# Kernel optimization log

Measured on AMD Instinct MI355X. Metric: run time of the kernel, lower is better.

The kernel has to match this reference:

```python
import jax, jax.numpy as jnp
import numpy as np

N = 40000   # nodes
E = 600000  # edges
G = 64      # graphs
DIN = 128   # input feature dim
H = 128     # hidden_channels
L = 3       # num_layers


def setup_inputs() -> dict:
    key = jax.random.key(0)
    ks = jax.random.split(key, 16)
    s = 0.05
    inp = {}
    inp["x"] = jax.random.normal(ks[0], (N, DIN), jnp.float32)
    inp["edge_attr"] = jax.random.normal(ks[1], (E,), jnp.float32)
    inp["node_w"] = jax.random.normal(ks[2], (DIN, H), jnp.float32) * s
    inp["node_b"] = jnp.zeros((H,), jnp.float32)
    inp["edge_w"] = jax.random.normal(ks[3], (1, H), jnp.float32) * s
    inp["edge_b"] = jnp.zeros((H,), jnp.float32)
    inp["t"] = jnp.ones((L,), jnp.float32)  # learn_t init 1.0
    inp["lin1_w"] = jax.random.normal(ks[4], (L, H, 2 * H), jnp.float32) * s
    inp["lin1_b"] = jnp.zeros((L, 2 * H), jnp.float32)
    inp["ln1_g"] = jnp.ones((L, 2 * H), jnp.float32)
    inp["ln1_bt"] = jnp.zeros((L, 2 * H), jnp.float32)
    inp["lin2_w"] = jax.random.normal(ks[5], (L, 2 * H, H), jnp.float32) * s
    inp["lin2_b"] = jnp.zeros((L, H), jnp.float32)
    inp["blk_g"] = jnp.ones((L, H), jnp.float32)
    inp["blk_b"] = jnp.zeros((L, H), jnp.float32)
    inp["hw1"] = jax.random.normal(ks[6], (H, H // 2), jnp.float32) * s
    inp["hb1"] = jnp.zeros((H // 2,), jnp.float32)
    inp["hw2"] = jax.random.normal(ks[7], (H // 2, H // 4), jnp.float32) * s
    inp["hb2"] = jnp.zeros((H // 4,), jnp.float32)
    inp["hw3"] = jax.random.normal(ks[8], (H // 4, 1), jnp.float32) * s
    inp["hb3"] = jnp.zeros((1,), jnp.float32)
    inp["edge_index"] = jax.random.randint(ks[9], (2, E), 0, N, jnp.int32)
    inp["batch"] = jnp.sort(jax.random.randint(ks[10], (N,), 0, G, jnp.int32))
    return inp


def _layer_norm(v, g, b):
    mu = jnp.mean(v, axis=-1, keepdims=True)
    var = jnp.var(v, axis=-1, keepdims=True)
    return (v - mu) * jax.lax.rsqrt(var + 1e-5) * g + b


def reference(x, edge_attr, node_w, node_b, edge_w, edge_b, t,
              lin1_w, lin1_b, ln1_g, ln1_bt, lin2_w, lin2_b,
              blk_g, blk_b, hw1, hb1, hw2, hb2, hw3, hb3,
              edge_index, batch):
    src, dst = edge_index[0], edge_index[1]
    h = x @ node_w + node_b                       # [N, H]
    ea = edge_attr[:, None] @ edge_w + edge_b     # [E, H]

    def genconv(xn, i):
        # message: relu(x_j + e) + eps
        msg = jax.nn.relu(xn[src] + ea) + 1e-7    # [E, H]
        # scatter-softmax over dst with learnable temperature t
        logit = msg * t[i]
        m = jax.ops.segment_max(logit, dst, num_segments=N)
        m = jnp.where(jnp.isfinite(m), m, 0.0)    # isolated nodes
        ex = jnp.exp(logit - m[dst])
        den = jax.ops.segment_sum(ex, dst, num_segments=N)
        agg = jax.ops.segment_sum(ex * msg, dst, num_segments=N) / jnp.maximum(den, 1e-16)
        o = agg + xn                              # add root
        # GENConv MLP: Linear(H,2H) -> LayerNorm -> ReLU -> Linear(2H,H)
        o = jax.nn.relu(_layer_norm(o @ lin1_w[i] + lin1_b[i], ln1_g[i], ln1_bt[i]))
        return o @ lin2_w[i] + lin2_b[i]

    # layer 0: bare conv (as in the torch forward)
    h = genconv(h, 0)
    # layers 1..L-1: DeepGCNLayer res+ (norm -> act -> [dropout=id in eval] -> conv -> residual)
    for i in range(1, L):
        r = jax.nn.relu(_layer_norm(h, blk_g[i], blk_b[i]))
        h = h + genconv(r, i)
    # final norm+act uses layer 0's norm/act
    h = jax.nn.relu(_layer_norm(h, blk_g[0], blk_b[0]))
    # global mean pool over graphs
    cnt = jax.ops.segment_sum(jnp.ones((N,), h.dtype), batch, num_segments=G)
    pooled = jax.ops.segment_sum(h, batch, num_segments=G) / jnp.maximum(cnt, 1.0)[:, None]
    # MLP head (dropout = identity in eval)
    o = jax.nn.relu(pooled @ hw1 + hb1)
    o = jax.nn.relu(o @ hw2 + hb2)
    return o @ hw3 + hb3                          # [G, 1]
```

## Files before the change

kernel.cpp:

```cpp
#include <hip/hip_runtime.h>
#include <math.h>

#define NN 40000
#define NE 600000
#define NG 64
#define DIM_IN 128
#define HH 128
#define HH2 256

using half8 = __attribute__((ext_vector_type(8))) _Float16;
using half4 = __attribute__((ext_vector_type(4))) _Float16;
using h2    = __attribute__((ext_vector_type(2))) _Float16;
using f4    = __attribute__((ext_vector_type(4))) float;

__device__ __forceinline__ int lower_bound_dev(const int* a, int n, int key) {
    int lo = 0, hi = n;
    while (lo < hi) { int mid = (lo + hi) >> 1; if (a[mid] < key) lo = mid + 1; else hi = mid; }
    return lo;
}

#define NX (NN*DIM_IN)
#define NX4 (NX/4)
__global__ void convert_kernel(const float* __restrict__ x, const float* __restrict__ node_w,
                               const float* __restrict__ lin1_w, const float* __restrict__ lin2_w,
                               _Float16* __restrict__ xh, _Float16* __restrict__ nwt,
                               _Float16* __restrict__ w1t, _Float16* __restrict__ w2t)
{
    int id = blockIdx.x * blockDim.x + threadIdx.x;
    if (id < NX4) {
        float4 v = *(const float4*)(x + (size_t)id * 4);
        half4 o; o.x = (_Float16)v.x; o.y = (_Float16)v.y; o.z = (_Float16)v.z; o.w = (_Float16)v.w;
        *(half4*)(xh + (size_t)id * 4) = o;
        return;
    }
    id -= NX4;
    if (id < 16384) { int n = id >> 7, k = id & 127; nwt[id] = (_Float16)node_w[k*128 + n]; return; }
    id -= 16384;
    if (id < 98304) {
        int l = id >> 15, r = id & 32767;
        int n = r >> 7, k = r & 127;
        w1t[id] = (_Float16)lin1_w[l*32768 + k*256 + n];
        return;
    }
    id -= 98304;
    if (id < 98304) {
        int l = id >> 15, r = id & 32767;
        int n = r >> 8, k = r & 255;
        w2t[id] = (_Float16)lin2_w[l*32768 + k*128 + n];
    }
}

__global__ void count_rank_kernel(const int* __restrict__ dst, int* __restrict__ counts,
                                  int* __restrict__ rank) {
    int e = blockIdx.x * blockDim.x + threadIdx.x;
    if (e < NE) rank[e] = atomicAdd(&counts[dst[e]], 1);
}

__global__ __launch_bounds__(1024) void scanA_kernel(const int* __restrict__ counts,
                                                     int* __restrict__ tmp, int* __restrict__ btot) {
    __shared__ int wpre[16];
    int t = threadIdx.x, lane = t & 63, wid = t >> 6;
    int i = blockIdx.x * 1024 + t;
    int v = (i < NN) ? counts[i] : 0;
    int s = v;
    #pragma unroll
    for (int off = 1; off < 64; off <<= 1) {
        int u = __shfl_up(s, off, 64);
        if (lane >= off) s += u;
    }
    if (lane == 63) wpre[wid] = s;
    __syncthreads();
    if (t == 0) {
        int run = 0;
        #pragma unroll
        for (int j = 0; j < 16; ++j) { int xv = wpre[j]; wpre[j] = run; run += xv; }
        btot[blockIdx.x] = run;
    }
    __syncthreads();
    if (i < NN) tmp[i] = s + wpre[wid];
}

__global__ __launch_bounds__(64) void scanB_kernel(const int* __restrict__ btot,
                                                   int* __restrict__ boff, int nb) {
    int t = threadIdx.x;
    int v = (t < nb) ? btot[t] : 0;
    int s = v;
    #pragma unroll
    for (int off = 1; off < 64; off <<= 1) {
        int u = __shfl_up(s, off, 64);
        if (t >= off) s += u;
    }
    if (t < nb) boff[t] = s - v;
}

__global__ __launch_bounds__(1024) void scanC_kernel(const int* __restrict__ tmp,
                                                     const int* __restrict__ boff,
                                                     int* __restrict__ rowp) {
    int i = blockIdx.x * 1024 + threadIdx.x;
    if (i < NN) rowp[i + 1] = tmp[i] + boff[blockIdx.x];
    if (i == 0) rowp[0] = 0;
}

__global__ void fill2_kernel(const int* __restrict__ src, const int* __restrict__ dst,
                             const float* __restrict__ eattr, const int* __restrict__ rowp,
                             const int* __restrict__ rank, int2* __restrict__ rec) {
    int e = blockIdx.x * blockDim.x + threadIdx.x;
    if (e < NE) {
        int pos = rowp[dst[e]] + rank[e];
        rec[pos] = make_int2(src[e], __float_as_int(eattr[e]));
    }
}

__global__ __launch_bounds__(256) void agg_kernel(
    const _Float16* __restrict__ xh,
    const int* __restrict__ row_ptr,
    const int2* __restrict__ rec,
    const float* __restrict__ ew, const float* __restrict__ eb,
    const float* __restrict__ tptr, int layer,
    _Float16* __restrict__ oh)
{
    int d = blockIdx.x * 4 + (threadIdx.x >> 6);
    int lane = threadIdx.x & 63;
    int c0 = 2 * lane;
    float tc = tptr[layer];
    float ew0 = ew[c0], eb0 = eb[c0];
    float ew1 = ew[c0 + 1], eb1 = eb[c0 + 1];
    int beg = row_ptr[d], end = row_ptr[d + 1];
    float den0 = 0.f, num0 = 0.f, den1 = 0.f, num1 = 0.f;
    for (int base = beg; base < end; base += 64) {
        int cnt = min(64, end - base);
        int2 mv = rec[base + min(lane, cnt - 1)];
        int sv = mv.x;
        float av = __int_as_float(mv.y);
        h2 gA[8], gB[8]; float aA[8], aB[8];
        auto issue = [&](h2 (&g)[8], float (&aa)[8], int j0) {
            #pragma unroll
            for (int u = 0; u < 8; ++u) {
                int jj = min(j0 + u, cnt - 1);
                int s = __shfl(sv, jj, 64);
                aa[u] = __shfl(av, jj, 64);
                g[u] = *(const h2*)(xh + ((size_t)s << 7) + c0);
            }
        };
        auto consume = [&](h2 (&g)[8], float (&aa)[8], int j0) {
            int lim = min(8, cnt - j0);
            #pragma unroll
            for (int u = 0; u < 8; ++u) {
                if (u < lim) {
                    float m0 = fmaxf(__fmaf_rn(aa[u], ew0, eb0) + (float)g[u].x, 0.f) + 1e-7f;
                    float m1 = fmaxf(__fmaf_rn(aa[u], ew1, eb1) + (float)g[u].y, 0.f) + 1e-7f;
                    float e0 = __expf(m0 * tc), e1 = __expf(m1 * tc);
                    den0 += e0; num0 = __fmaf_rn(e0, m0, num0);
                    den1 += e1; num1 = __fmaf_rn(e1, m1, num1);
                }
            }
        };
        issue(gA, aA, 0);
        for (int j0 = 0; j0 < cnt; j0 += 16) {
            if (j0 + 8 < cnt)  issue(gB, aB, j0 + 8);
            consume(gA, aA, j0);
            if (j0 + 16 < cnt) issue(gA, aA, j0 + 16);
            if (j0 + 8 < cnt)  consume(gB, aB, j0 + 8);
        }
    }
    h2 sv2 = *(const h2*)(xh + ((size_t)d << 7) + c0);
    float o0 = num0 / fmaxf(den0, 1e-16f) + (float)sv2.x;
    float o1 = num1 / fmaxf(den1, 1e-16f) + (float)sv2.y;
    h2 ov; ov.x = (_Float16)o0; ov.y = (_Float16)o1;
    *(h2*)(oh + ((size_t)d << 7) + c0) = ov;
}

__global__ __launch_bounds__(256) void gemm_mfma(
    const _Float16* __restrict__ A, const _Float16* __restrict__ Bt,
    const float* __restrict__ bias, _Float16* __restrict__ C,
    int M, int N, int K)
{
    constexpr int LDA = 40;
    __shared__ _Float16 As[64 * LDA];
    __shared__ _Float16 Bs[128 * LDA];
    int t = threadIdx.x;
    int row0 = blockIdx.y * 64;
    int col0 = blockIdx.x * 128;
    int w = t >> 6, lane = t & 63;
    int wm = w & 1, wn = w >> 1;
    int q = lane >> 4, l16 = lane & 15;
    f4 acc[2][4];
    #pragma unroll
    for (int i = 0; i < 2; ++i)
        #pragma unroll
        for (int j = 0; j < 4; ++j)
            acc[i][j] = (f4){0.f, 0.f, 0.f, 0.f};

    for (int k0 = 0; k0 < K; k0 += 32) {
        {
            int r = t >> 2, seg = t & 3;
            *(float4*)&As[r * LDA + seg * 8] =
                *(const float4*)(A + (size_t)(row0 + r) * K + k0 + seg * 8);
        }
        #pragma unroll
        for (int i = 0; i < 2; ++i) {
            int idx = t + i * 256;
            int r = idx >> 2, seg = idx & 3;
            *(float4*)&Bs[r * LDA + seg * 8] =
                *(const float4*)(Bt + (size_t)(col0 + r) * K + k0 + seg * 8);
        }
        __syncthreads();
        half8 af[2], bf[4];
        #pragma unroll
        for (int i = 0; i < 2; ++i)
            af[i] = *(const half8*)&As[(wm * 32 + i * 16 + l16) * LDA + q * 8];
        #pragma unroll
        for (int j = 0; j < 4; ++j)
            bf[j] = *(const half8*)&Bs[(wn * 64 + j * 16 + l16) * LDA + q * 8];
        #pragma unroll
        for (int i = 0; i < 2; ++i)
            #pragma unroll
            for (int j = 0; j < 4; ++j)
                acc[i][j] = __builtin_amdgcn_mfma_f32_16x16x32_f16(af[i], bf[j], acc[i][j], 0, 0, 0);
        __syncthreads();
    }
    #pragma unroll
    for (int j = 0; j < 4; ++j) {
        int col = col0 + wn * 64 + j * 16 + l16;
        float bv = bias[col];
        #pragma unroll
        for (int i = 0; i < 2; ++i) {
            int rbase = row0 + wm * 32 + i * 16 + q * 4;
            #pragma unroll
            for (int rg = 0; rg < 4; ++rg)
                C[(size_t)(rbase + rg) * N + col] = (_Float16)(acc[i][j][rg] + bv);
        }
    }
}

template<int RES>
__global__ __launch_bounds__(256) void mlp_fused(
    const _Float16* __restrict__ Ain,
    const _Float16* __restrict__ w1t,
    const float* __restrict__ b1,
    const float* __restrict__ g1, const float* __restrict__ bt1,
    const _Float16* __restrict__ w2t,
    const float* __restrict__ b2,
    float* __restrict__ h,
    const float* __restrict__ bg, const float* __restrict__ bb,
    _Float16* __restrict__ xout)
{
    constexpr int LDA = 136;
    constexpr int LDB = 40;
    constexpr int LDM = 264;
    __shared__ _Float16 As[64 * LDA];
    __shared__ _Float16 Bs[256 * LDB];
    __shared__ _Float16 midh[64 * LDM];
    __shared__ float ssum[64][2], ssum2[64][2];
    int t = threadIdx.x;
    int row0 = blockIdx.x * 64;
    int w = t >> 6, lane = t & 63;
    int wm = w & 1, wn = w >> 1;
    int q = lane >> 4, l16 = lane & 15;

    #pragma unroll
    for (int p = 0; p < 4; ++p) {
        int idx = t + p * 256;
        int r = idx >> 4, seg = idx & 15;
        *(float4*)&As[r * LDA + seg * 8] =
            *(const float4*)(Ain + (size_t)(row0 + r) * 128 + seg * 8);
    }

    f4 acc[2][8];
    #pragma unroll
    for (int i = 0; i < 2; ++i)
        #pragma unroll
        for (int j = 0; j < 8; ++j)
            acc[i][j] = (f4){0.f, 0.f, 0.f, 0.f};
    for (int k0 = 0; k0 < 128; k0 += 32) {
        #pragma unroll
        for (int p = 0; p < 4; ++p) {
            int idx = t + p * 256;
            int r = idx >> 2, seg = idx & 3;
            *(float4*)&Bs[r * LDB + seg * 8] =
                *(const float4*)(w1t + (size_t)r * 128 + k0 + seg * 8);
        }
        __syncthreads();
        half8 af[2], bf[8];
        #pragma unroll
        for (int i = 0; i < 2; ++i)
            af[i] = *(const half8*)&As[(wm * 32 + i * 16 + l16) * LDA + k0 + q * 8];
        #pragma unroll
        for (int j = 0; j < 8; ++j)
            bf[j] = *(const half8*)&Bs[(wn * 128 + j * 16 + l16) * LDB + q * 8];
        #pragma unroll
        for (int i = 0; i < 2; ++i)
            #pragma unroll
            for (int j = 0; j < 8; ++j)
                acc[i][j] = __builtin_amdgcn_mfma_f32_16x16x32_f16(af[i], bf[j], acc[i][j], 0, 0, 0);
        __syncthreads();
    }

    float b1v[8], g1v[8], bt1v[8];
    #pragma unroll
    for (int j = 0; j < 8; ++j) {
        int col = wn * 128 + j * 16 + l16;
        b1v[j] = b1[col]; g1v[j] = g1[col]; bt1v[j] = bt1[col];
    }
    float vals[2][8][4];
    #pragma unroll
    for (int i = 0; i < 2; ++i)
        #pragma unroll
        for (int j = 0; j < 8; ++j)
            #pragma unroll
            for (int rg = 0; rg < 4; ++rg)
                vals[i][j][rg] = acc[i][j][rg] + b1v[j];
    #pragma unroll
    for (int i = 0; i < 2; ++i) {
        #pragma unroll
        for (int rg = 0; rg < 4; ++rg) {
            float ps = 0.f, ps2 = 0.f;
            #pragma unroll
            for (int j = 0; j < 8; ++j) { float v = vals[i][j][rg]; ps += v; ps2 += v * v; }
            #pragma unroll
            for (int off = 1; off < 16; off <<= 1) {
                ps  += __shfl_xor(ps,  off, 16);
                ps2 += __shfl_xor(ps2, off, 16);
            }
            if (l16 == 0) {
                int row = wm * 32 + i * 16 + q * 4 + rg;
                ssum[row][wn] = ps; ssum2[row][wn] = ps2;
            }
        }
    }
    __syncthreads();
    #pragma unroll
    for (int i = 0; i < 2; ++i) {
        #pragma unroll
        for (int rg = 0; rg < 4; ++rg) {
            int row = wm * 32 + i * 16 + q * 4 + rg;
            float S = ssum[row][0] + ssum[row][1];
            float S2 = ssum2[row][0] + ssum2[row][1];
            float mu = S * (1.0f / 256.0f);
            float var = S2 * (1.0f / 256.0f) - mu * mu;
            float rstd = rsqrtf(var + 1e-5f);
            #pragma unroll
            for (int j = 0; j < 8; ++j) {
                int col = wn * 128 + j * 16 + l16;
                float o = fmaxf((vals[i][j][rg] - mu) * rstd * g1v[j] + bt1v[j], 0.f);
                midh[row * LDM + col] = (_Float16)o;
            }
        }
    }
    __syncthreads();

    f4 acc2[2][4];
    #pragma unroll
    for (int i = 0; i < 2; ++i)
        #pragma unroll
        for (int j = 0; j < 4; ++j)
            acc2[i][j] = (f4){0.f, 0.f, 0.f, 0.f};
    for (int k0 = 0; k0 < 256; k0 += 32) {
        #pragma unroll
        for (int p = 0; p < 2; ++p) {
            int idx = t + p * 256;
            int r = idx >> 2, seg = idx & 3;
            *(float4*)&Bs[r * LDB + seg * 8] =
                *(const float4*)(w2t + (size_t)r * 256 + k0 + seg * 8);
        }
        __syncthreads();
        half8 af2[2], bf2[4];
        #pragma unroll
        for (int i = 0; i < 2; ++i)
            af2[i] = *(const half8*)&midh[(wm * 32 + i * 16 + l16) * LDM + k0 + q * 8];
        #pragma unroll
        for (int j = 0; j < 4; ++j)
            bf2[j] = *(const half8*)&Bs[(wn * 64 + j * 16 + l16) * LDB + q * 8];
        #pragma unroll
        for (int i = 0; i < 2; ++i)
            #pragma unroll
            for (int j = 0; j < 4; ++j)
                acc2[i][j] = __builtin_amdgcn_mfma_f32_16x16x32_f16(af2[i], bf2[j], acc2[i][j], 0, 0, 0);
        __syncthreads();
    }

    float b2v[4], bgv[4], bbv[4];
    #pragma unroll
    for (int j = 0; j < 4; ++j) {
        int col = wn * 64 + j * 16 + l16;
        b2v[j] = b2[col]; bgv[j] = bg[col]; bbv[j] = bb[col];
    }
    float ov[2][4][4];
    #pragma unroll
    for (int i = 0; i < 2; ++i) {
        #pragma unroll
        for (int rg = 0; rg < 4; ++rg) {
            int row = wm * 32 + i * 16 + q * 4 + rg;
            #pragma unroll
            for (int j = 0; j < 4; ++j) {
                int col = wn * 64 + j * 16 + l16;
                float v = acc2[i][j][rg] + b2v[j];
                size_t gidx = (size_t)(row0 + row) * 128 + col;
                if (RES) v += h[gidx];
                h[gidx] = v;
                ov[i][j][rg] = v;
            }
        }
    }
    #pragma unroll
    for (int i = 0; i < 2; ++i) {
        #pragma unroll
        for (int rg = 0; rg < 4; ++rg) {
            float ps = 0.f, ps2 = 0.f;
            #pragma unroll
            for (int j = 0; j < 4; ++j) { float v = ov[i][j][rg]; ps += v; ps2 += v * v; }
            #pragma unroll
            for (int off = 1; off < 16; off <<= 1) {
                ps  += __shfl_xor(ps,  off, 16);
                ps2 += __shfl_xor(ps2, off, 16);
            }
            if (l16 == 0) {
                int row = wm * 32 + i * 16 + q * 4 + rg;
                ssum[row][wn] = ps; ssum2[row][wn] = ps2;
            }
        }
    }
    __syncthreads();
    #pragma unroll
    for (int i = 0; i < 2; ++i) {
        #pragma unroll
        for (int rg = 0; rg < 4; ++rg) {
            int row = wm * 32 + i * 16 + q * 4 + rg;
            float S = ssum[row][0] + ssum[row][1];
            float S2 = ssum2[row][0] + ssum2[row][1];
            float mu = S * (1.0f / 128.0f);
            float var = S2 * (1.0f / 128.0f) - mu * mu;
            float rstd = rsqrtf(var + 1e-5f);
            #pragma unroll
            for (int j = 0; j < 4; ++j) {
                int col = wn * 64 + j * 16 + l16;
                float o = fmaxf((ov[i][j][rg] - mu) * rstd * bgv[j] + bbv[j], 0.f);
                xout[(size_t)(row0 + row) * 128 + col] = (_Float16)o;
            }
        }
    }
}

__global__ __launch_bounds__(128) void pool_kernel(
    const _Float16* __restrict__ f, const int* __restrict__ batch, float* __restrict__ pooled)
{
    int g = blockIdx.x;
    int chunk = blockIdx.y;
    int c = threadIdx.x;
    int s = lower_bound_dev(batch, NN, g);
    int e = lower_bound_dev(batch, NN, g + 1);
    int len = e - s;
    if (len <= 0) return;
    int nch = gridDim.y;
    int per = (len + nch - 1) / nch;
    int cs = s + chunk * per;
    int ce = min(cs + per, e);
    if (cs >= ce) return;
    float acc = 0.f;
    for (int n = cs; n < ce; ++n) acc += (float)f[(size_t)n * HH + c];
    atomicAdd(&pooled[g * HH + c], acc);
}

__global__ __launch_bounds__(128) void head_kernel(
    const float* __restrict__ pooled, const int* __restrict__ batch,
    const float* __restrict__ hw1, const float* __restrict__ hb1,
    const float* __restrict__ hw2, const float* __restrict__ hb2,
    const float* __restrict__ hw3, const float* __restrict__ hb3,
    float* __restrict__ out)
{
    __shared__ float p[HH];
    __shared__ float o1[64];
    __shared__ float o2[32];
    int g = blockIdx.x;
    int t = threadIdx.x;
    int s = lower_bound_dev(batch, NN, g);
    int e = lower_bound_dev(batch, NN, g + 1);
    float cnt = fmaxf((float)(e - s), 1.0f);
    p[t] = pooled[g * HH + t] / cnt;
    __syncthreads();
    if (t < 64) {
        float acc = hb1[t];
        for (int k = 0; k < HH; ++k) acc += p[k] * hw1[k * 64 + t];
        o1[t] = fmaxf(acc, 0.f);
    }
    __syncthreads();
    if (t < 32) {
        float acc = hb2[t];
        for (int k = 0; k < 64; ++k) acc += o1[k] * hw2[k * 32 + t];
        o2[t] = fmaxf(acc, 0.f);
    }
    __syncthreads();
    if (t == 0) {
        float acc = hb3[0];
        for (int k = 0; k < 32; ++k) acc += o2[k] * hw3[k];
        out[g] = acc;
    }
}

extern "C" void kernel_launch(void* const* d_in, const int* in_sizes, int n_in,
                              void* d_out, int out_size, void* d_ws, size_t ws_size,
                              hipStream_t stream)
{
    const float* x      = (const float*)d_in[0];
    const float* eattr  = (const float*)d_in[1];
    const float* node_w = (const float*)d_in[2];
    const float* node_b = (const float*)d_in[3];
    const float* edge_w = (const float*)d_in[4];
    const float* edge_b = (const float*)d_in[5];
    const float* tptr   = (const float*)d_in[6];
    const float* lin1_w = (const float*)d_in[7];
    const float* lin1_b = (const float*)d_in[8];
    const float* ln1_g  = (const float*)d_in[9];
    const float* ln1_bt = (const float*)d_in[10];
    const float* lin2_w = (const float*)d_in[11];
    const float* lin2_b = (const float*)d_in[12];
    const float* blk_g  = (const float*)d_in[13];
    const float* blk_b  = (const float*)d_in[14];
    const float* hw1    = (const float*)d_in[15];
    const float* hb1    = (const float*)d_in[16];
    const float* hw2    = (const float*)d_in[17];
    const float* hb2    = (const float*)d_in[18];
    const float* hw3    = (const float*)d_in[19];
    const float* hb3    = (const float*)d_in[20];
    const int*   eidx   = (const int*)d_in[21];
    const int*   batch  = (const int*)d_in[22];
    const int* src = eidx;
    const int* dst = eidx + NE;
    float* out = (float*)d_out;

    char* ws = (char*)d_ws;
    size_t off = 0;
    auto carve = [&](size_t bytes) -> char* {
        char* p = ws + off;
        off = (off + bytes + 255) & ~(size_t)255;
        return p;
    };
    float*    h      = (float*)carve((size_t)NN * HH * 4);
    _Float16* xh_in  = (_Float16*)carve((size_t)NX * 2);
    _Float16* xnh    = (_Float16*)carve((size_t)NN * HH * 2);
    _Float16* oh     = (_Float16*)carve((size_t)NN * HH * 2);
    _Float16* rh     = (_Float16*)carve((size_t)NN * HH * 2);
    _Float16* nwt    = (_Float16*)carve((size_t)16384 * 2);
    _Float16* w1t    = (_Float16*)carve((size_t)98304 * 2);
    _Float16* w2t    = (_Float16*)carve((size_t)98304 * 2);
    int*      counts = (int*)carve((size_t)NN * 4);
    int*      rank   = (int*)carve((size_t)NE * 4);
    int*      tmp    = (int*)carve((size_t)NN * 4);
    int*      btot   = (int*)carve((size_t)64 * 4);
    int*      boff   = (int*)carve((size_t)64 * 4);
    int*      rowp   = (int*)carve((size_t)(NN + 1) * 4);
    int2*     rec    = (int2*)carve((size_t)NE * 8);
    float*    pooled = (float*)carve((size_t)NG * HH * 4);

    hipMemsetAsync(counts, 0, (size_t)NN * 4, stream);
    hipMemsetAsync(pooled, 0, (size_t)NG * HH * 4, stream);

    {
        int total = NX4 + 16384 + 98304 + 98304;
        convert_kernel<<<(total + 255) / 256, 256, 0, stream>>>(
            x, node_w, lin1_w, lin2_w, xh_in, nwt, w1t, w2t);
    }
    const int NB = (NN + 1023) / 1024;
    count_rank_kernel<<<(NE + 255) / 256, 256, 0, stream>>>(dst, counts, rank);
    scanA_kernel<<<NB, 1024, 0, stream>>>(counts, tmp, btot);
    scanB_kernel<<<1, 64, 0, stream>>>(btot, boff, NB);
    scanC_kernel<<<NB, 1024, 0, stream>>>(tmp, boff, rowp);
    fill2_kernel<<<(NE + 255) / 256, 256, 0, stream>>>(src, dst, eattr, rowp, rank, rec);

    gemm_mfma<<<dim3(1, NN / 64), 256, 0, stream>>>(xh_in, nwt, node_b, xnh, NN, HH, DIM_IN);

    agg_kernel<<<NN / 4, 256, 0, stream>>>(xnh, rowp, rec, edge_w, edge_b, tptr, 0, oh);
    mlp_fused<0><<<NN / 64, 256, 0, stream>>>(
        oh, w1t, lin1_b, ln1_g, ln1_bt, w2t, lin2_b,
        h, blk_g + 1 * HH, blk_b + 1 * HH, xnh);
    agg_kernel<<<NN / 4, 256, 0, stream>>>(xnh, rowp, rec, edge_w, edge_b, tptr, 1, oh);
    mlp_fused<1><<<NN / 64, 256, 0, stream>>>(
        oh, w1t + 32768, lin1_b + HH2, ln1_g + HH2, ln1_bt + HH2, w2t + 32768, lin2_b + HH,
        h, blk_g + 2 * HH, blk_b + 2 * HH, xnh);
    agg_kernel<<<NN / 4, 256, 0, stream>>>(xnh, rowp, rec, edge_w, edge_b, tptr, 2, oh);
    mlp_fused<1><<<NN / 64, 256, 0, stream>>>(
        oh, w1t + 2 * 32768, lin1_b + 2 * HH2, ln1_g + 2 * HH2, ln1_bt + 2 * HH2,
        w2t + 2 * 32768, lin2_b + 2 * HH,
        h, blk_g, blk_b, rh);

    pool_kernel<<<dim3(NG, 8), 128, 0, stream>>>(rh, batch, pooled);
    head_kernel<<<NG, 128, 0, stream>>>(pooled, batch, hw1, hb1, hw2, hb2, hw3, hb3, out);
}
```

Baseline: 394.0 us.

## Fuse edge aggregation into per-layer MLP kernel and merge setup kernels

The softmax aggregation is moved into the MLP kernel, so each wave aggregates 16 consecutive destination nodes straight into the shared-memory A tile. This removes the oh round trip through global memory and three kernel launches. Ping-pong xa/xb buffers are used so one layer's output does not overwrite the input still being gathered by other blocks. Count/rank and the pooled-buffer zeroing are folded into the convert kernel, and scanB is merged into scanC with a per-block reduction. Shared memory is reused between As and midh with an XOR swizzle, which trades occupancy and per-block parallelism (NN/64 blocks instead of NN/4) for less memory traffic.

```diff
diff --git a/kernel.cpp b/kernel.cpp
--- a/kernel.cpp
+++ b/kernel.cpp
@@ -23,6 +23,8 @@
 #define NX4 (NX/4)
 __global__ void convert_kernel(const float* __restrict__ x, const float* __restrict__ node_w,
                                const float* __restrict__ lin1_w, const float* __restrict__ lin2_w,
+                               const int* __restrict__ dst, int* __restrict__ counts,
+                               int* __restrict__ rank, float* __restrict__ pooled,
                                _Float16* __restrict__ xh, _Float16* __restrict__ nwt,
                                _Float16* __restrict__ w1t, _Float16* __restrict__ w2t)
 {
@@ -47,13 +49,12 @@
         int l = id >> 15, r = id & 32767;
         int n = r >> 8, k = r & 255;
         w2t[id] = (_Float16)lin2_w[l*32768 + k*128 + n];
-    }
-}
-
-__global__ void count_rank_kernel(const int* __restrict__ dst, int* __restrict__ counts,
-                                  int* __restrict__ rank) {
-    int e = blockIdx.x * blockDim.x + threadIdx.x;
-    if (e < NE) rank[e] = atomicAdd(&counts[dst[e]], 1);
+        return;
+    }
+    id -= 98304;
+    if (id < NG * HH) { pooled[id] = 0.f; return; }
+    id -= NG * HH;
+    if (id < NE) rank[id] = atomicAdd(&counts[dst[id]], 1);
 }
 
 __global__ __launch_bounds__(1024) void scanA_kernel(const int* __restrict__ counts,
@@ -80,24 +81,20 @@
     if (i < NN) tmp[i] = s + wpre[wid];
 }
 
-__global__ __launch_bounds__(64) void scanB_kernel(const int* __restrict__ btot,
-                                                   int* __restrict__ boff, int nb) {
+__global__ __launch_bounds__(1024) void scanC_kernel(const int* __restrict__ tmp,
+                                                     const int* __restrict__ btot,
+                                                     int* __restrict__ rowp) {
+    __shared__ int s_off;
     int t = threadIdx.x;
-    int v = (t < nb) ? btot[t] : 0;
-    int s = v;
-    #pragma unroll
-    for (int off = 1; off < 64; off <<= 1) {
-        int u = __shfl_up(s, off, 64);
-        if (t >= off) s += u;
-    }
-    if (t < nb) boff[t] = s - v;
-}
-
-__global__ __launch_bounds__(1024) void scanC_kernel(const int* __restrict__ tmp,
-                                                     const int* __restrict__ boff,
-                                                     int* __restrict__ rowp) {
-    int i = blockIdx.x * 1024 + threadIdx.x;
-    if (i < NN) rowp[i + 1] = tmp[i] + boff[blockIdx.x];
+    if (t < 64) {
+        int v = (t < blockIdx.x) ? btot[t] : 0;
+        #pragma unroll
+        for (int o = 32; o > 0; o >>= 1) v += __shfl_down(v, o, 64);
+        if (t == 0) s_off = v;
+    }
+    __syncthreads();
+    int i = blockIdx.x * 1024 + t;
+    if (i < NN) rowp[i + 1] = tmp[i] + s_off;
     if (i == 0) rowp[0] = 0;
 }
 
@@ -109,65 +106,6 @@
         int pos = rowp[dst[e]] + rank[e];
         rec[pos] = make_int2(src[e], __float_as_int(eattr[e]));
     }
-}
-
-__global__ __launch_bounds__(256) void agg_kernel(
-    const _Float16* __restrict__ xh,
-    const int* __restrict__ row_ptr,
-    const int2* __restrict__ rec,
-    const float* __restrict__ ew, const float* __restrict__ eb,
-    const float* __restrict__ tptr, int layer,
-    _Float16* __restrict__ oh)
-{
-    int d = blockIdx.x * 4 + (threadIdx.x >> 6);
-    int lane = threadIdx.x & 63;
-    int c0 = 2 * lane;
-    float tc = tptr[layer];
-    float ew0 = ew[c0], eb0 = eb[c0];
-    float ew1 = ew[c0 + 1], eb1 = eb[c0 + 1];
-    int beg = row_ptr[d], end = row_ptr[d + 1];
-    float den0 = 0.f, num0 = 0.f, den1 = 0.f, num1 = 0.f;
-    for (int base = beg; base < end; base += 64) {
-        int cnt = min(64, end - base);
-        int2 mv = rec[base + min(lane, cnt - 1)];
-        int sv = mv.x;
-        float av = __int_as_float(mv.y);
-        h2 gA[8], gB[8]; float aA[8], aB[8];
-        auto issue = [&](h2 (&g)[8], float (&aa)[8], int j0) {
-            #pragma unroll
-            for (int u = 0; u < 8; ++u) {
-                int jj = min(j0 + u, cnt - 1);
-                int s = __shfl(sv, jj, 64);
-                aa[u] = __shfl(av, jj, 64);
-                g[u] = *(const h2*)(xh + ((size_t)s << 7) + c0);
-            }
-        };
-        auto consume = [&](h2 (&g)[8], float (&aa)[8], int j0) {
-            int lim = min(8, cnt - j0);
-            #pragma unroll
-            for (int u = 0; u < 8; ++u) {
-                if (u < lim) {
-                    float m0 = fmaxf(__fmaf_rn(aa[u], ew0, eb0) + (float)g[u].x, 0.f) + 1e-7f;
-                    float m1 = fmaxf(__fmaf_rn(aa[u], ew1, eb1) + (float)g[u].y, 0.f) + 1e-7f;
-                    float e0 = __expf(m0 * tc), e1 = __expf(m1 * tc);
-                    den0 += e0; num0 = __fmaf_rn(e0, m0, num0);
-                    den1 += e1; num1 = __fmaf_rn(e1, m1, num1);
-                }
-            }
-        };
-        issue(gA, aA, 0);
-        for (int j0 = 0; j0 < cnt; j0 += 16) {
-            if (j0 + 8 < cnt)  issue(gB, aB, j0 + 8);
-            consume(gA, aA, j0);
-            if (j0 + 16 < cnt) issue(gA, aA, j0 + 16);
-            if (j0 + 8 < cnt)  consume(gB, aB, j0 + 8);
-        }
-    }
-    h2 sv2 = *(const h2*)(xh + ((size_t)d << 7) + c0);
-    float o0 = num0 / fmaxf(den0, 1e-16f) + (float)sv2.x;
-    float o1 = num1 / fmaxf(den1, 1e-16f) + (float)sv2.y;
-    h2 ov; ov.x = (_Float16)o0; ov.y = (_Float16)o1;
-    *(h2*)(oh + ((size_t)d << 7) + c0) = ov;
 }
 
 __global__ __launch_bounds__(256) void gemm_mfma(
@@ -234,36 +172,111 @@
 }
 
 template<int RES>
-__global__ __launch_bounds__(256) void mlp_fused(
-    const _Float16* __restrict__ Ain,
-    const _Float16* __restrict__ w1t,
-    const float* __restrict__ b1,
+__global__ __launch_bounds__(256) void layer_fused(
+    const _Float16* __restrict__ xh,
+    const int* __restrict__ rowp,
+    const int2* __restrict__ rec,
+    const float* __restrict__ ew, const float* __restrict__ eb,
+    const float* __restrict__ tptr, int layer,
+    const _Float16* __restrict__ w1t, const float* __restrict__ b1,
     const float* __restrict__ g1, const float* __restrict__ bt1,
-    const _Float16* __restrict__ w2t,
-    const float* __restrict__ b2,
+    const _Float16* __restrict__ w2t, const float* __restrict__ b2,
     float* __restrict__ h,
     const float* __restrict__ bg, const float* __restrict__ bb,
     _Float16* __restrict__ xout)
 {
     constexpr int LDA = 136;
     constexpr int LDB = 40;
-    constexpr int LDM = 264;
-    __shared__ _Float16 As[64 * LDA];
-    __shared__ _Float16 Bs[256 * LDB];
-    __shared__ _Float16 midh[64 * LDM];
-    __shared__ float ssum[64][2], ssum2[64][2];
+    __shared__ __align__(16) char smem[54272];
+    _Float16* As   = (_Float16*)smem;
+    _Float16* midh = (_Float16*)smem;
+    _Float16* Bs   = (_Float16*)(smem + 32768);
+    float* ssum    = (float*)(smem + 53248);
+    float* ssum2   = (float*)(smem + 53760);
+
     int t = threadIdx.x;
     int row0 = blockIdx.x * 64;
     int w = t >> 6, lane = t & 63;
     int wm = w & 1, wn = w >> 1;
     int q = lane >> 4, l16 = lane & 15;
-
-    #pragma unroll
-    for (int p = 0; p < 4; ++p) {
-        int idx = t + p * 256;
-        int r = idx >> 4, seg = idx & 15;
-        *(float4*)&As[r * LDA + seg * 8] =
-            *(const float4*)(Ain + (size_t)(row0 + r) * 128 + seg * 8);
+    int c0 = 2 * lane;
+
+    {
+        int d0 = row0 + w * 16;
+        float tc = tptr[layer];
+        float ew0 = ew[c0], eb0 = eb[c0];
+        float ew1 = ew[c0 + 1], eb1 = eb[c0 + 1];
+        #pragma unroll
+        for (int i = 0; i < 16; ++i) {
+            h2 rt = *(const h2*)(xh + ((size_t)(d0 + i) << 7) + c0);
+            *(h2*)&As[(w * 16 + i) * LDA + c0] = rt;
+        }
+        int rp_l = rowp[d0 + min(lane, 16)];
+        int beg = __shfl(rp_l, 0, 64);
+        int end = __shfl(rp_l, 16, 64);
+        int total = end - beg;
+        int cur = 0;
+        int nb_rel = __shfl(rp_l, 1, 64) - beg;
+        float den0 = 0.f, num0 = 0.f, den1 = 0.f, num1 = 0.f;
+
+        auto finalize = [&]() {
+            float o0 = num0 / fmaxf(den0, 1e-16f);
+            float o1 = num1 / fmaxf(den1, 1e-16f);
+            h2* slot = (h2*)&As[(w * 16 + cur) * LDA + c0];
+            h2 old = *slot;
+            h2 nv; nv.x = (_Float16)((float)old.x + o0); nv.y = (_Float16)((float)old.y + o1);
+            *slot = nv;
+            den0 = num0 = den1 = num1 = 0.f;
+            cur++;
+            nb_rel = __shfl(rp_l, min(cur + 1, 16), 64) - beg;
+        };
+
+        if (total > 0) {
+            int ms = 0; float ma = 0.f;
+            auto load_chunk = [&](int ci) {
+                int jj = min(ci * 64 + lane, total - 1);
+                int2 mv = rec[beg + jj];
+                ms = mv.x; ma = __int_as_float(mv.y);
+            };
+            h2 gA[16], gB[16]; float aA[16], aB[16];
+            auto issue = [&](h2* g, float* aa, int g0) {
+                #pragma unroll
+                for (int u = 0; u < 16; ++u) {
+                    int jl = min(g0 + u, total - 1) & 63;
+                    int s = __shfl(ms, jl, 64);
+                    aa[u] = __shfl(ma, jl, 64);
+                    g[u] = *(const h2*)(xh + ((size_t)s << 7) + c0);
+                }
+            };
+            auto consume = [&](h2* g, float* aa, int g0) {
+                #pragma unroll
+                for (int u = 0; u < 16; ++u) {
+                    int p = g0 + u;
+                    if (p < total) {
+                        while (cur < 16 && p == nb_rel) finalize();
+                        float m0 = fmaxf(__fmaf_rn(aa[u], ew0, eb0) + (float)g[u].x, 0.f) + 1e-7f;
+                        float m1 = fmaxf(__fmaf_rn(aa[u], ew1, eb1) + (float)g[u].y, 0.f) + 1e-7f;
+                        float e0 = __expf(m0 * tc), e1 = __expf(m1 * tc);
+                        den0 += e0; num0 = __fmaf_rn(e0, m0, num0);
+                        den1 += e1; num1 = __fmaf_rn(e1, m1, num1);
+                    }
+                }
+            };
+            load_chunk(0);
+            issue(gA, aA, 0);
+            int ng = (total + 15) >> 4;
+            for (int gi = 0; gi < ng; ++gi) {
+                int gn = gi + 1;
+                if (gn < ng) {
+                    if ((gn & 3) == 0) load_chunk(gn >> 2);
+                    if (gi & 1) issue(gA, aA, gn << 4);
+                    else        issue(gB, aB, gn << 4);
+                }
+                if (gi & 1) consume(gB, aB, gi << 4);
+                else        consume(gA, aA, gi << 4);
+            }
+        }
+        while (cur < 16) finalize();
     }
 
     f4 acc[2][8];
@@ -324,7 +337,7 @@
             }
             if (l16 == 0) {
                 int row = wm * 32 + i * 16 + q * 4 + rg;
-                ssum[row][wn] = ps; ssum2[row][wn] = ps2;
+                ssum[row * 2 + wn] = ps; ssum2[row * 2 + wn] = ps2;
             }
         }
     }
@@ -334,8 +347,8 @@
         #pragma unroll
         for (int rg = 0; rg < 4; ++rg) {
             int row = wm * 32 + i * 16 + q * 4 + rg;
-            float S = ssum[row][0] + ssum[row][1];
-            float S2 = ssum2[row][0] + ssum2[row][1];
+            float S = ssum[row * 2 + 0] + ssum[row * 2 + 1];
+            float S2 = ssum2[row * 2 + 0] + ssum2[row * 2 + 1];
             float mu = S * (1.0f / 256.0f);
             float var = S2 * (1.0f / 256.0f) - mu * mu;
             float rstd = rsqrtf(var + 1e-5f);
@@ -343,7 +356,8 @@
             for (int j = 0; j < 8; ++j) {
                 int col = wn * 128 + j * 16 + l16;
                 float o = fmaxf((vals[i][j][rg] - mu) * rstd * g1v[j] + bt1v[j], 0.f);
-                midh[row * LDM + col] = (_Float16)o;
+                int pg = (col >> 3) ^ (row & 31);
+                midh[row * 256 + (pg << 3) + (col & 7)] = (_Float16)o;
             }
         }
     }
@@ -366,8 +380,11 @@
         __syncthreads();
         half8 af2[2], bf2[4];
         #pragma unroll
-        for (int i = 0; i < 2; ++i)
-            af2[i] = *(const half8*)&midh[(wm * 32 + i * 16 + l16) * LDM + k0 + q * 8];
+        for (int i = 0; i < 2; ++i) {
+            int rr = wm * 32 + i * 16 + l16;
+            int pg = ((k0 >> 3) + q) ^ (rr & 31);
+            af2[i] = *(const half8*)&midh[rr * 256 + (pg << 3)];
+        }
         #pragma unroll
         for (int j = 0; j < 4; ++j)
             bf2[j] = *(const half8*)&Bs[(wn * 64 + j * 16 + l16) * LDB + q * 8];
@@ -416,7 +433,7 @@
             }
             if (l16 == 0) {
                 int row = wm * 32 + i * 16 + q * 4 + rg;
-                ssum[row][wn] = ps; ssum2[row][wn] = ps2;
+                ssum[row * 2 + wn] = ps; ssum2[row * 2 + wn] = ps2;
             }
         }
     }
@@ -426,8 +443,8 @@
         #pragma unroll
         for (int rg = 0; rg < 4; ++rg) {
             int row = wm * 32 + i * 16 + q * 4 + rg;
-            float S = ssum[row][0] + ssum[row][1];
-            float S2 = ssum2[row][0] + ssum2[row][1];
+            float S = ssum[row * 2 + 0] + ssum[row * 2 + 1];
+            float S2 = ssum2[row * 2 + 0] + ssum2[row * 2 + 1];
             float mu = S * (1.0f / 128.0f);
             float var = S2 * (1.0f / 128.0f) - mu * mu;
             float rstd = rsqrtf(var + 1e-5f);
@@ -537,8 +554,8 @@
     };
     float*    h      = (float*)carve((size_t)NN * HH * 4);
     _Float16* xh_in  = (_Float16*)carve((size_t)NX * 2);
-    _Float16* xnh    = (_Float16*)carve((size_t)NN * HH * 2);
-    _Float16* oh     = (_Float16*)carve((size_t)NN * HH * 2);
+    _Float16* xa     = (_Float16*)carve((size_t)NN * HH * 2);
+    _Float16* xb     = (_Float16*)carve((size_t)NN * HH * 2);
     _Float16* rh     = (_Float16*)carve((size_t)NN * HH * 2);
     _Float16* nwt    = (_Float16*)carve((size_t)16384 * 2);
     _Float16* w1t    = (_Float16*)carve((size_t)98304 * 2);
@@ -547,39 +564,35 @@
     int*      rank   = (int*)carve((size_t)NE * 4);
     int*      tmp    = (int*)carve((size_t)NN * 4);
     int*      btot   = (int*)carve((size_t)64 * 4);
-    int*      boff   = (int*)carve((size_t)64 * 4);
     int*      rowp   = (int*)carve((size_t)(NN + 1) * 4);
     int2*     rec    = (int2*)carve((size_t)NE * 8);
     float*    pooled = (float*)carve((size_t)NG * HH * 4);
 
     hipMemsetAsync(counts, 0, (size_t)NN * 4, stream);
-    hipMemsetAsync(pooled, 0, (size_t)NG * HH * 4, stream);
 
     {
-        int total = NX4 + 16384 + 98304 + 98304;
+        int total = NX4 + 16384 + 98304 + 98304 + NG * HH + NE;
         convert_kernel<<<(total + 255) / 256, 256, 0, stream>>>(
-            x, node_w, lin1_w, lin2_w, xh_in, nwt, w1t, w2t);
+            x, node_w, lin1_w, lin2_w, dst, counts, rank, pooled, xh_in, nwt, w1t, w2t);
     }
     const int NB = (NN + 1023) / 1024;
-    count_rank_kernel<<<(NE + 255) / 256, 256, 0, stream>>>(dst, counts, rank);
     scanA_kernel<<<NB, 1024, 0, stream>>>(counts, tmp, btot);
-    scanB_kernel<<<1, 64, 0, stream>>>(btot, boff, NB);
-    scanC_kernel<<<NB, 1024, 0, stream>>>(tmp, boff, rowp);
+    scanC_kernel<<<NB, 1024, 0, stream>>>(tmp, btot, rowp);
     fill2_kernel<<<(NE + 255) / 256, 256, 0, stream>>>(src, dst, eattr, rowp, rank, rec);
 
-    gemm_mfma<<<dim3(1, NN / 64), 256, 0, stream>>>(xh_in, nwt, node_b, xnh, NN, HH, DIM_IN);
-
-    agg_kernel<<<NN / 4, 256, 0, stream>>>(xnh, rowp, rec, edge_w, edge_b, tptr, 0, oh);
-    mlp_fused<0><<<NN / 64, 256, 0, stream>>>(
-        oh, w1t, lin1_b, ln1_g, ln1_bt, w2t, lin2_b,
-        h, blk_g + 1 * HH, blk_b + 1 * HH, xnh);
-    agg_kernel<<<NN / 4, 256, 0, stream>>>(xnh, rowp, rec, edge_w, edge_b, tptr, 1, oh);
-    mlp_fused<1><<<NN / 64, 256, 0, stream>>>(
-        oh, w1t + 32768, lin1_b + HH2, ln1_g + HH2, ln1_bt + HH2, w2t + 32768, lin2_b + HH,
-        h, blk_g + 2 * HH, blk_b + 2 * HH, xnh);
-    agg_kernel<<<NN / 4, 256, 0, stream>>>(xnh, rowp, rec, edge_w, edge_b, tptr, 2, oh);
-    mlp_fused<1><<<NN / 64, 256, 0, stream>>>(
-        oh, w1t + 2 * 32768, lin1_b + 2 * HH2, ln1_g + 2 * HH2, ln1_bt + 2 * HH2,
+    gemm_mfma<<<dim3(1, NN / 64), 256, 0, stream>>>(xh_in, nwt, node_b, xa, NN, HH, DIM_IN);
+
+    layer_fused<0><<<NN / 64, 256, 0, stream>>>(
+        xa, rowp, rec, edge_w, edge_b, tptr, 0,
+        w1t, lin1_b, ln1_g, ln1_bt, w2t, lin2_b,
+        h, blk_g + 1 * HH, blk_b + 1 * HH, xb);
+    layer_fused<1><<<NN / 64, 256, 0, stream>>>(
+        xb, rowp, rec, edge_w, edge_b, tptr, 1,
+        w1t + 32768, lin1_b + HH2, ln1_g + HH2, ln1_bt + HH2, w2t + 32768, lin2_b + HH,
+        h, blk_g + 2 * HH, blk_b + 2 * HH, xa);
+    layer_fused<1><<<NN / 64, 256, 0, stream>>>(
+        xa, rowp, rec, edge_w, edge_b, tptr, 2,
+        w1t + 2 * 32768, lin1_b + 2 * HH2, ln1_g + 2 * HH2, ln1_bt + 2 * HH2,
         w2t + 2 * 32768, lin2_b + 2 * HH,
         h, blk_g, blk_b, rh);
 
```

Result: slower. 516.2 us (+31.0%).
